# Performance work log

Measured on AMD Instinct MI355X. Metric: run time of the kernel, lower is better.

Reference implementation:

```python
import jax, jax.numpy as jnp
import numpy as np

B, S, H, V, T, NS, NB, NSW = 16, 200, 400, 25000, 8, 30, 3, 36


def setup_inputs() -> dict:
    key = jax.random.key(0)
    ks = jax.random.split(key, 12)
    return {
        "encoded_hidden": jax.random.normal(ks[0], (1, B, H), jnp.float32),
        "encoded_outputs": jax.random.normal(ks[1], (B, S, H), jnp.float32),
        "story": jax.random.randint(ks[2], (B, S), 0, V),
        "target_batches": jax.random.randint(ks[3], (B, NS, T), 0, V),
        "slot_dom_idx": jax.random.randint(ks[4], (NS,), 0, NSW),
        "slot_slot_idx": jax.random.randint(ks[5], (NS,), 0, NSW),
        "emb_W": jax.random.normal(ks[6], (V, H), jnp.float32) * 0.05,
        "slot_emb_W": jax.random.normal(ks[7], (NSW, H), jnp.float32) * 0.1,
        "gru_W_ih": jax.random.normal(ks[8], (3 * H, H), jnp.float32) * 0.05,
        "gru_W_hh": jax.random.normal(ks[9], (3 * H, H), jnp.float32) * 0.05,
        "gru_b_ih": jnp.zeros((3 * H,), jnp.float32),
        "gru_b_hh": jnp.zeros((3 * H,), jnp.float32),
        "W_ratio_w": jax.random.normal(ks[10], (1, 3 * H), jnp.float32) * 0.05,
        "W_ratio_b": jnp.zeros((1,), jnp.float32),
        "W_gate_w": jax.random.normal(ks[11], (NB, H), jnp.float32) * 0.05,
        "W_gate_b": jnp.zeros((NB,), jnp.float32),
    }


def reference(encoded_hidden, encoded_outputs, story, target_batches,
              slot_dom_idx, slot_slot_idx, emb_W, slot_emb_W,
              gru_W_ih, gru_W_hh, gru_b_ih, gru_b_hh,
              W_ratio_w, W_ratio_b, W_gate_w, W_gate_b):
    b, s, h = encoded_outputs.shape
    ns = slot_dom_idx.shape[0]
    v = emb_W.shape[0]
    t = target_batches.shape[2]
    bs = ns * b  # flattened slot*batch dim (parallel decode over slots)

    # slot embedding = domain_emb + slot_emb, broadcast over batch
    slot_emb = slot_emb_W[slot_dom_idx] + slot_emb_W[slot_slot_idx]        # [ns,h]
    dec_in0 = jnp.broadcast_to(slot_emb[:, None, :], (ns, b, h)).reshape(bs, h)
    h0 = jnp.tile(encoded_hidden[0], (ns, 1))                              # [bs,h]
    enc = jnp.tile(encoded_outputs, (ns, 1, 1))                            # [bs,s,h]
    pad_mask = jnp.tile(story == 0, (ns, 1))                               # [bs,s]
    story_rep = jnp.tile(story, (ns, 1))                                   # [bs,s]
    # teacher forcing targets, slot-major flatten: [bs, t]
    tf = jnp.transpose(target_batches, (1, 0, 2)).reshape(bs, t)
    rows = jnp.arange(bs)

    def gru_cell(x, hid):
        gx = x @ gru_W_ih.T + gru_b_ih
        gh = hid @ gru_W_hh.T + gru_b_hh
        r = jax.nn.sigmoid(gx[:, :h] + gh[:, :h])
        z = jax.nn.sigmoid(gx[:, h:2 * h] + gh[:, h:2 * h])
        n = jnp.tanh(gx[:, 2 * h:] + r * gh[:, 2 * h:])
        return (1.0 - z) * n + z * hid

    def step(carry, tgt_t):
        hid, x = carry
        hid = gru_cell(x, hid)                                             # [bs,h]
        scores = jnp.einsum('bh,bsh->bs', hid, enc)
        scores = jnp.where(pad_mask, -jnp.inf, scores)
        prob = jax.nn.softmax(scores, axis=1)                              # [bs,s]
        ctx = jnp.einsum('bs,bsh->bh', prob, enc)                          # [bs,h]
        p_vocab = jax.nn.softmax(hid @ emb_W.T, axis=1)                    # [bs,v]
        switch = jax.nn.sigmoid(
            jnp.concatenate([hid, ctx, x], axis=-1) @ W_ratio_w.T + W_ratio_b)  # [bs,1]
        p_ctx = jnp.zeros((bs, v), p_vocab.dtype).at[rows[:, None], story_rep].add(prob)
        final = (1.0 - switch) * p_ctx + switch * p_vocab                  # [bs,v]
        x_next = emb_W[tgt_t]                                              # teacher forcing
        return (hid, x_next), (final, ctx)

    (_, _), (finals, ctxs) = jax.lax.scan(step, (h0, dec_in0), tf.T)
    all_point = jnp.transpose(finals.reshape(t, ns, b, v), (1, 2, 0, 3))   # [ns,b,t,v]
    all_gate = (ctxs[0] @ W_gate_w.T + W_gate_b).reshape(ns, b, -1)        # [ns,b,nb_gate]
    return all_point, all_gate
```

## Files before the change

### kernel.cpp

```cpp
#include <hip/hip_runtime.h>
#include <math.h>

#define B_   16
#define S_   200
#define H_   400
#define V_   25000
#define T_   8
#define NS_  30
#define NB_  3
#define NSW_ 36
#define BS_  480

#define KP_  448
#define MP_  512
#define NP_  25088
#define NG_  1280
#define MA_  3840
#define NVT_ (NP_/128)
#define PSL_ 200

typedef unsigned short u16;
typedef __attribute__((ext_vector_type(4))) float f32x4;
typedef __attribute__((ext_vector_type(8))) short short8;

__device__ __forceinline__ u16 f2bf(float f) {
    unsigned u = __float_as_uint(f);
    u += 0x7FFFu + ((u >> 16) & 1u);
    return (u16)(u >> 16);
}
__device__ __forceinline__ float bf2f(u16 v) {
    return __uint_as_float(((unsigned)v) << 16);
}
__device__ __forceinline__ float wred_sum(float v) {
    v += __shfl_xor(v, 32); v += __shfl_xor(v, 16); v += __shfl_xor(v, 8);
    v += __shfl_xor(v, 4);  v += __shfl_xor(v, 2);  v += __shfl_xor(v, 1);
    return v;
}
__device__ __forceinline__ float wred_max(float v) {
    v = fmaxf(v, __shfl_xor(v, 32)); v = fmaxf(v, __shfl_xor(v, 16));
    v = fmaxf(v, __shfl_xor(v, 8));  v = fmaxf(v, __shfl_xor(v, 4));
    v = fmaxf(v, __shfl_xor(v, 2));  v = fmaxf(v, __shfl_xor(v, 1));
    return v;
}

__device__ __forceinline__ void gload_lds16(const void* g, void* l) {
    __builtin_amdgcn_global_load_lds(
        (const __attribute__((address_space(1))) void*)g,
        (__attribute__((address_space(3))) void*)l, 16, 0, 0);
}

#define MFMA_SETUP()                                                          \
    const int wid = tid >> 6, lane = tid & 63;                                \
    const int wr = wid >> 1, wc = wid & 1;                                    \
    f32x4 acc[4][4] = {};                                                     \
    const int sslot = lane & 7;                                               \
    const int srow8 = (lane >> 3) & 7;                                        \
    const int lcol = (sslot ^ srow8) * 8;                                     \
    const int lr = lane & 15, lg = lane >> 4, lx = lane & 7;                  \
    const int sA0 = (lg ^ lx) * 8, sA1 = ((4 + lg) ^ lx) * 8;

#define STAGE_TILE(k0_)                                                       \
    {                                                                         \
        _Pragma("unroll")                                                     \
        for (int is = 0; is < 4; ++is) {                                      \
            gload_lds16(Ag + (size_t)is * 8 * KP_ + (k0_),                    \
                        &As[(wid * 32 + is * 8) * 64]);                       \
            gload_lds16(Bg + (size_t)is * 8 * KP_ + (k0_),                    \
                        &Bs[(wid * 32 + is * 8) * 64]);                       \
        }                                                                     \
    }

#define COMPUTE_TILE()                                                        \
    {                                                                         \
        short8 af[4][2], bfr[4][2];                                           \
        _Pragma("unroll")                                                     \
        for (int i = 0; i < 4; ++i) {                                         \
            int ra = (wr * 64 + i * 16 + lr) * 64;                            \
            af[i][0] = *reinterpret_cast<const short8*>(&As[ra + sA0]);       \
            af[i][1] = *reinterpret_cast<const short8*>(&As[ra + sA1]);       \
            int rb = (wc * 64 + i * 16 + lr) * 64;                            \
            bfr[i][0] = *reinterpret_cast<const short8*>(&Bs[rb + sA0]);      \
            bfr[i][1] = *reinterpret_cast<const short8*>(&Bs[rb + sA1]);      \
        }                                                                     \
        _Pragma("unroll")                                                     \
        for (int h = 0; h < 2; ++h)                                           \
            _Pragma("unroll")                                                 \
            for (int i = 0; i < 4; ++i)                                       \
                _Pragma("unroll")                                             \
                for (int j = 0; j < 4; ++j)                                   \
                    acc[i][j] = __builtin_amdgcn_mfma_f32_16x16x32_bf16(      \
                        af[i][h], bfr[j][h], acc[i][j], 0, 0, 0);             \
    }

#define MFMA_KLOOP_SB()                                                       \
    _Pragma("unroll")                                                         \
    for (int kt = 0; kt < 7; ++kt) {                                          \
        STAGE_TILE(kt * 64);                                                  \
        __syncthreads();                                                      \
        COMPUTE_TILE();                                                       \
        __syncthreads();                                                      \
    }

__global__ void init_all(const float* __restrict__ eh, float* __restrict__ hid,
                         u16* __restrict__ Ab) {
    int i = blockIdx.x * blockDim.x + threadIdx.x;
    if (i >= MP_ * KP_) return;
    int row = i / KP_, d = i - row * KP_;
    u16 v = 0;
    if (row < BS_ && d < H_) {
        float h = eh[(row % B_) * H_ + d];
        hid[row * H_ + d] = h;
        v = f2bf(h);
    }
    Ab[i] = v;
}

__device__ __forceinline__ void conv_chunk(const float* __restrict__ src,
                                           u16* __restrict__ dst, int i, int rows) {
    int row = i / (KP_ / 8), c8 = (i - row * (KP_ / 8)) * 8;
    short8 o = {};
    if (row < rows && c8 < H_) {
        const float4* s = reinterpret_cast<const float4*>(src + (size_t)row * H_ + c8);
        float4 a = s[0], b = s[1];
        o[0] = (short)f2bf(a.x); o[1] = (short)f2bf(a.y);
        o[2] = (short)f2bf(a.z); o[3] = (short)f2bf(a.w);
        o[4] = (short)f2bf(b.x); o[5] = (short)f2bf(b.y);
        o[6] = (short)f2bf(b.z); o[7] = (short)f2bf(b.w);
    }
    *reinterpret_cast<short8*>(dst + (size_t)row * KP_ + c8) = o;
}

__global__ void conv_all(const float* __restrict__ embW, const float* __restrict__ Wih,
                         const float* __restrict__ Whh, u16* __restrict__ Bb,
                         u16* __restrict__ Wihb, u16* __restrict__ Whhb) {
    const int CB = NP_ * (KP_ / 8), CG = NG_ * (KP_ / 8);
    int i = blockIdx.x * blockDim.x + threadIdx.x;
    if (i < CB) conv_chunk(embW, Bb, i, V_);
    else if (i < CB + CG) conv_chunk(Wih, Wihb, i - CB, 3 * H_);
    else if (i < CB + 2 * CG) conv_chunk(Whh, Whhb, i - CB - CG, 3 * H_);
}

__global__ void xall_prep(const int* __restrict__ tb, const float* __restrict__ embW,
                          const float* __restrict__ sembW,
                          const int* __restrict__ dom, const int* __restrict__ sli,
                          float* __restrict__ x_all, u16* __restrict__ Xb_all) {
    int i = blockIdx.x * blockDim.x + threadIdx.x;
    if (i >= MA_ * (KP_ / 8)) return;
    int row = i / (KP_ / 8), c8 = (i - row * (KP_ / 8)) * 8;
    int t = row / BS_, r = row - t * BS_;
    int batch = r % B_, slot = r / B_;
    short8 o = {};
    if (c8 < H_) {
        float4 a, b;
        if (t == 0) {
            const float4* s0 = reinterpret_cast<const float4*>(sembW + dom[slot] * H_ + c8);
            const float4* s1 = reinterpret_cast<const float4*>(sembW + sli[slot] * H_ + c8);
            float4 x0 = s0[0], x1 = s0[1], y0 = s1[0], y1 = s1[1];
            a = make_float4(x0.x + y0.x, x0.y + y0.y, x0.z + y0.z, x0.w + y0.w);
            b = make_float4(x1.x + y1.x, x1.y + y1.y, x1.z + y1.z, x1.w + y1.w);
        } else {
            int tok = tb[(batch * NS_ + slot) * T_ + (t - 1)];
            const float4* s = reinterpret_cast<const float4*>(embW + (size_t)tok * H_ + c8);
            a = s[0]; b = s[1];
        }
        o[0] = (short)f2bf(a.x); o[1] = (short)f2bf(a.y);
        o[2] = (short)f2bf(a.z); o[3] = (short)f2bf(a.w);
        o[4] = (short)f2bf(b.x); o[5] = (short)f2bf(b.y);
        o[6] = (short)f2bf(b.z); o[7] = (short)f2bf(b.w);
        *reinterpret_cast<float4*>(x_all + (size_t)row * H_ + c8) = a;
        *reinterpret_cast<float4*>(x_all + (size_t)row * H_ + c8 + 4) = b;
    }
    *reinterpret_cast<short8*>(Xb_all + (size_t)row * KP_ + c8) = o;
}

__global__ __launch_bounds__(256)
void gemm_setup(const u16* __restrict__ Xb_all, const u16* __restrict__ Abuf,
                const u16* __restrict__ Wihb, const u16* __restrict__ Whhb,
                float* __restrict__ gx_all, float* __restrict__ gh) {
    __shared__ u16 As[128 * 64];
    __shared__ u16 Bs[128 * 64];
    const int tid = threadIdx.x;
    const bool mainp = blockIdx.y < (MA_ / 128);
    const int m0 = (mainp ? blockIdx.y : blockIdx.y - MA_ / 128) * 128;
    const int n0 = blockIdx.x * 128;
    const u16* A = mainp ? Xb_all : Abuf;
    const u16* Bw = mainp ? Wihb : Whhb;
    float* C = mainp ? gx_all : gh;
    const int Mlim = mainp ? MA_ : BS_;

    MFMA_SETUP();
    const u16* Ag = A + (size_t)(m0 + wid * 32 + (lane >> 3)) * KP_ + lcol;
    const u16* Bg = Bw + (size_t)(n0 + wid * 32 + (lane >> 3)) * KP_ + lcol;
    MFMA_KLOOP_SB();

    const int m_base = m0 + wr * 64 + lg * 4;
    const int n_base = n0 + wc * 64 + lr;
    #pragma unroll
    for (int i = 0; i < 4; ++i)
        #pragma unroll
        for (int r = 0; r < 4; ++r) {
            int m = m_base + i * 16 + r;
            if (m >= Mlim) continue;
            #pragma unroll
            for (int j = 0; j < 4; ++j) {
                int n = n_base + j * 16;
                if (n < 3 * H_) C[(size_t)m * 3 * H_ + n] = acc[i][j][r];
            }
        }
}

__global__ __launch_bounds__(256)
void vocab_gh(const u16* __restrict__ A, const u16* __restrict__ Bb,
              const u16* __restrict__ Whhb, u16* __restrict__ pb_cur,
              float* __restrict__ psum_cur, float* __restrict__ gh,
              const u16* __restrict__ pb_prev, const float* __restrict__ psum_prev,
              const float* __restrict__ sw_prev, const float* __restrict__ prob_prev,
              const int* __restrict__ story, float* __restrict__ out,
              int t, int do_fin) {
    __shared__ u16 As[128 * 64];
    __shared__ u16 Bs[128 * 64];
    __shared__ float sred[2][128];
    const int bid = blockIdx.x;
    const int tid = threadIdx.x;

    if (do_fin && t > 0 && bid < BS_) {
        const int row = bid, batch = row % B_;
        const int w = tid >> 6, l = tid & 63;
        float rs = (tid < NVT_) ? psum_prev[(size_t)row * PSL_ + tid] : 0.f;
        rs = wred_sum(rs);
        if (l == 0) sred[0][w] = rs;
        __syncthreads();
        float denom = sred[0][0] + sred[0][1] + sred[0][2] + sred[0][3];
        float swv = sw_prev[row];
        float scl = swv / denom;
        const u16* ps = pb_prev + (size_t)row * V_;
        float* p = out + ((size_t)row * T_ + (t - 1)) * V_;
        for (int v = tid * 8; v < V_; v += 256 * 8) {
            short8 in = *reinterpret_cast<const short8*>(ps + v);
            float4 o0, o1;
            o0.x = bf2f((u16)in[0]) * scl; o0.y = bf2f((u16)in[1]) * scl;
            o0.z = bf2f((u16)in[2]) * scl; o0.w = bf2f((u16)in[3]) * scl;
            o1.x = bf2f((u16)in[4]) * scl; o1.y = bf2f((u16)in[5]) * scl;
            o1.z = bf2f((u16)in[6]) * scl; o1.w = bf2f((u16)in[7]) * scl;
            *reinterpret_cast<float4*>(p + v) = o0;
            *reinterpret_cast<float4*>(p + v + 4) = o1;
        }
        __syncthreads();
        float om = 1.f - swv;
        for (int s = tid; s < S_; s += 256) {
            int tok = story[batch * S_ + s];
            atomicAdd(p + tok, om * prob_prev[(size_t)row * S_ + s]);
        }
        __syncthreads();
    }

    const int lin = (bid & 7) * 103 + (bid >> 3);
    const int ntall = lin >> 2, mt = lin & 3;
    const bool isv = (ntall < NVT_);
    const int n0 = (isv ? ntall : ntall - NVT_) * 128;
    const int m0 = mt * 128;
    const u16* Bsrc = isv ? Bb : Whhb;

    MFMA_SETUP();
    const u16* Ag = A + (size_t)(m0 + wid * 32 + (lane >> 3)) * KP_ + lcol;
    const u16* Bg = Bsrc + (size_t)(n0 + wid * 32 + (lane >> 3)) * KP_ + lcol;
    MFMA_KLOOP_SB();

    const int m_base = m0 + wr * 64 + lg * 4;
    const int n_base = n0 + wc * 64 + lr;
    if (isv) {
        #pragma unroll
        for (int i = 0; i < 4; ++i) {
            #pragma unroll
            for (int r = 0; r < 4; ++r) {
                int m = m_base + i * 16 + r;
                float js = 0.f;
                #pragma unroll
                for (int j = 0; j < 4; ++j) {
                    int n = n_base + j * 16;
                    float e = __expf(acc[i][j][r]);
                    if (m < BS_ && n < V_) {
                        pb_cur[(size_t)m * V_ + n] = f2bf(e);
                        js += e;
                    }
                }
                js += __shfl_xor(js, 1);
                js += __shfl_xor(js, 2);
                js += __shfl_xor(js, 4);
                js += __shfl_xor(js, 8);
                if ((lane & 15) == 0) sred[wc][m - m0] = js;
            }
        }
        __syncthreads();
        if (tid < 128) {
            int m = m0 + tid;
            psum_cur[(size_t)m * PSL_ + ntall] = sred[0][tid] + sred[1][tid];
        }
    } else {
        #pragma unroll
        for (int i = 0; i < 4; ++i)
            #pragma unroll
            for (int r = 0; r < 4; ++r) {
                int m = m_base + i * 16 + r;
                if (m >= BS_) continue;
                #pragma unroll
                for (int j = 0; j < 4; ++j) {
                    int n = n_base + j * 16;
                    if (n < 3 * H_) gh[(size_t)m * 3 * H_ + n] = acc[i][j][r];
                }
            }
    }
}

__global__ __launch_bounds__(256)
void attn_fused(const float* __restrict__ gx_all, const float* __restrict__ gh,
                const float* __restrict__ bih, const float* __restrict__ bhh,
                float* __restrict__ hid, u16* __restrict__ Ab,
                const float* __restrict__ x_all,
                const float* __restrict__ enc, const int* __restrict__ story,
                const float* __restrict__ Wr, const float* __restrict__ Wrb,
                const float* __restrict__ Wg, const float* __restrict__ Wgb,
                float* __restrict__ prob_cur, float* __restrict__ sw_cur,
                float* __restrict__ gate_out,
                float* __restrict__ out, const u16* __restrict__ pb_prev,
                const float* __restrict__ psum_prev, const float* __restrict__ sw_prev,
                const float* __restrict__ prob_prev, int t, int do_fin) {
    const int bid = blockIdx.x;
    const int lin = (bid & 7) * 60 + (bid >> 3);
    const int batch = lin / 30, slot = lin - batch * 30;
    const int row = slot * B_ + batch;
    const int tid = threadIdx.x, w = tid >> 6, l = tid & 63;
    __shared__ __align__(16) float hs[H_];
    __shared__ __align__(16) float xs[H_];
    __shared__ __align__(16) float cs[H_];
    __shared__ float sc[S_];
    __shared__ float red[16];

    if (do_fin && t > 0) {
        float rs = (tid < NVT_) ? psum_prev[(size_t)row * PSL_ + tid] : 0.f;
        rs = wred_sum(rs);
        if (l == 0) red[w] = rs;
        __syncthreads();
        float denom = red[0] + red[1] + red[2] + red[3];
        float swv = sw_prev[row];
        float scl = swv / denom;
        const u16* ps = pb_prev + (size_t)row * V_;
        float* p = out + ((size_t)row * T_ + (t - 1)) * V_;
        for (int v = tid * 8; v < V_; v += 256 * 8) {
            short8 in = *reinterpret_cast<const short8*>(ps + v);
            float4 o0, o1;
            o0.x = bf2f((u16)in[0]) * scl; o0.y = bf2f((u16)in[1]) * scl;
            o0.z = bf2f((u16)in[2]) * scl; o0.w = bf2f((u16)in[3]) * scl;
            o1.x = bf2f((u16)in[4]) * scl; o1.y = bf2f((u16)in[5]) * scl;
            o1.z = bf2f((u16)in[6]) * scl; o1.w = bf2f((u16)in[7]) * scl;
            *reinterpret_cast<float4*>(p + v) = o0;
            *reinterpret_cast<float4*>(p + v + 4) = o1;
        }
        __syncthreads();
        float om = 1.f - swv;
        for (int s = tid; s < S_; s += 256) {
            int tok = story[batch * S_ + s];
            atomicAdd(p + tok, om * prob_prev[(size_t)row * S_ + s]);
        }
        __syncthreads();
    }

    const float* gxr = gx_all + ((size_t)t * BS_ + row) * 3 * H_;
    const float* ghr = gh + (size_t)row * 3 * H_;
    const float* xr  = x_all + ((size_t)t * BS_ + row) * H_;
    for (int d = tid; d < H_; d += 256) {
        float r = 1.f / (1.f + expf(-(gxr[d] + bih[d] + ghr[d] + bhh[d])));
        float z = 1.f / (1.f + expf(-(gxr[H_ + d] + bih[H_ + d] + ghr[H_ + d] + bhh[H_ + d])));
        float n = tanhf(gxr[2 * H_ + d] + bih[2 * H_ + d] + r * (ghr[2 * H_ + d] + bhh[2 * H_ + d]));
        float h = (1.f - z) * n + z * hid[(size_t)row * H_ + d];
        hs[d] = h;
        hid[(size_t)row * H_ + d] = h;
        Ab[(size_t)row * KP_ + d] = f2bf(h);
        xs[d] = xr[d];
    }
    __syncthreads();

    const float* encb = enc + (size_t)batch * S_ * H_;
    {
        float4 hv1 = *reinterpret_cast<const float4*>(&hs[l * 4]);
        float4 hv2 = make_float4(0.f, 0.f, 0.f, 0.f);
        if (l < 36) hv2 = *reinterpret_cast<const float4*>(&hs[256 + l * 4]);
        for (int k = 0; k < 50; ++k) {
            int s = w * 50 + k;
            const float4* e = reinterpret_cast<const float4*>(encb + (size_t)s * H_);
            float4 ev = e[l];
            float part = ev.x * hv1.x + ev.y * hv1.y + ev.z * hv1.z + ev.w * hv1.w;
            if (l < 36) {
                float4 ev2 = e[64 + l];
                part += ev2.x * hv2.x + ev2.y * hv2.y + ev2.z * hv2.z + ev2.w * hv2.w;
            }
            part = wred_sum(part);
            if (l == 0)
                sc[s] = (story[batch * S_ + s] == 0) ? -1e30f : part;
        }
    }
    __syncthreads();

    float v = (tid < S_) ? sc[tid] : -1e30f;
    float wm = wred_max(v);
    if (l == 0) red[w] = wm;
    __syncthreads();
    float mx = fmaxf(fmaxf(red[0], red[1]), fmaxf(red[2], red[3]));
    float e = (tid < S_) ? __expf(v - mx) : 0.f;
    float wsum = wred_sum(e);
    if (l == 0) red[4 + w] = wsum;
    __syncthreads();
    float inv = 1.f / (red[4] + red[5] + red[6] + red[7]);
    if (tid < S_) {
        float pv = e * inv;
        sc[tid] = pv;
        prob_cur[(size_t)row * S_ + tid] = pv;
    }
    __syncthreads();

    for (int d = tid; d < H_; d += 256) {
        float a0 = 0.f, a1 = 0.f;
        for (int s = 0; s < S_; s += 2) {
            a0 += sc[s] * encb[(size_t)s * H_ + d];
            a1 += sc[s + 1] * encb[(size_t)(s + 1) * H_ + d];
        }
        cs[d] = a0 + a1;
    }
    __syncthreads();

    float part = 0.f;
    for (int i = tid; i < 3 * H_; i += 256) {
        float xv = (i < H_) ? hs[i] : (i < 2 * H_) ? cs[i - H_] : xs[i - 2 * H_];
        part += xv * Wr[i];
    }
    part = wred_sum(part);
    if (l == 0) red[8 + w] = part;
    __syncthreads();
    if (tid == 0)
        sw_cur[row] = 1.f / (1.f + expf(-(red[8] + red[9] + red[10] + red[11] + Wrb[0])));

    if (t == 0 && tid < NB_) {
        float acc = 0.f;
        for (int d = 0; d < H_; ++d) acc += cs[d] * Wg[tid * H_ + d];
        gate_out[(size_t)row * NB_ + tid] = acc + Wgb[tid];
    }
}

__global__ __launch_bounds__(256)
void scale_scatter(float* __restrict__ out, const u16* __restrict__ pb,
                   const float* __restrict__ psum, const float* __restrict__ sw,
                   const float* __restrict__ prob, const int* __restrict__ story) {
    const int row = blockIdx.x;
    const int tid = threadIdx.x, w = tid >> 6, l = tid & 63;
    __shared__ float red[4];
    float rs = (tid < NVT_) ? psum[(size_t)row * PSL_ + tid] : 0.f;
    rs = wred_sum(rs);
    if (l == 0) red[w] = rs;
    __syncthreads();
    float denom = red[0] + red[1] + red[2] + red[3];
    float swv = sw[row];
    float scl = swv / denom;
    const u16* ps = pb + (size_t)row * V_;
    float* p = out + ((size_t)row * T_ + (T_ - 1)) * V_;
    for (int v = tid * 8; v < V_; v += 256 * 8) {
        short8 in = *reinterpret_cast<const short8*>(ps + v);
        float4 o0, o1;
        o0.x = bf2f((u16)in[0]) * scl; o0.y = bf2f((u16)in[1]) * scl;
        o0.z = bf2f((u16)in[2]) * scl; o0.w = bf2f((u16)in[3]) * scl;
        o1.x = bf2f((u16)in[4]) * scl; o1.y = bf2f((u16)in[5]) * scl;
        o1.z = bf2f((u16)in[6]) * scl; o1.w = bf2f((u16)in[7]) * scl;
        *reinterpret_cast<float4*>(p + v) = o0;
        *reinterpret_cast<float4*>(p + v + 4) = o1;
    }
    __syncthreads();
    const int batch = row % B_;
    float om = 1.f - swv;
    for (int s = tid; s < S_; s += 256) {
        int tok = story[batch * S_ + s];
        atomicAdd(p + tok, om * prob[(size_t)row * S_ + s]);
    }
}

extern "C" void kernel_launch(void* const* d_in, const int* in_sizes, int n_in,
                              void* d_out, int out_size, void* d_ws, size_t ws_size,
                              hipStream_t stream) {
    const float* eh    = (const float*)d_in[0];
    const float* enc   = (const float*)d_in[1];
    const int*   story = (const int*)d_in[2];
    const int*   tb    = (const int*)d_in[3];
    const int*   dom   = (const int*)d_in[4];
    const int*   sli   = (const int*)d_in[5];
    const float* embW  = (const float*)d_in[6];
    const float* sembW = (const float*)d_in[7];
    const float* Wih   = (const float*)d_in[8];
    const float* Whh   = (const float*)d_in[9];
    const float* bih   = (const float*)d_in[10];
    const float* bhh   = (const float*)d_in[11];
    const float* Wr    = (const float*)d_in[12];
    const float* Wrb   = (const float*)d_in[13];
    const float* Wg    = (const float*)d_in[14];
    const float* Wgb   = (const float*)d_in[15];

    float* out = (float*)d_out;
    float* ws  = (float*)d_ws;

    float* gx_all = ws;
    float* gh     = gx_all + (size_t)MA_ * 3 * H_;
    float* hid    = gh + (size_t)BS_ * 3 * H_;
    float* x_all  = hid + (size_t)BS_ * H_;
    float* prob2  = x_all + (size_t)MA_ * H_;
    float* sw2    = prob2 + 2 * BS_ * S_;
    float* psum2  = sw2 + 2 * BS_;
    u16* Ab     = (u16*)(psum2 + 2 * (size_t)MP_ * PSL_);
    u16* Xb_all = Ab + (size_t)MP_ * KP_;
    u16* Wihb   = Xb_all + (size_t)MA_ * KP_;
    u16* Whhb   = Wihb + (size_t)NG_ * KP_;
    u16* Bb     = Whhb + (size_t)NG_ * KP_;
    u16* pb0    = Bb + (size_t)NP_ * KP_;
    u16* pb1    = pb0 + (size_t)BS_ * V_;
    size_t need_base = (size_t)((char*)pb1 - (char*)ws);
    size_t need_full = (size_t)((char*)(pb1 + (size_t)BS_ * V_) - (char*)ws);
    if (ws_size < need_base) return;
    const int dbl = (ws_size >= need_full) ? 1 : 0;

    float* gate_out = out + (size_t)NS_ * B_ * T_ * V_;

    init_all<<<(MP_ * KP_ + 255) / 256, 256, 0, stream>>>(eh, hid, Ab);
    {
        int tot = (NP_ + 2 * NG_) * (KP_ / 8);
        conv_all<<<(tot + 255) / 256, 256, 0, stream>>>(embW, Wih, Whh, Bb, Wihb, Whhb);
    }
    xall_prep<<<(MA_ * (KP_ / 8) + 255) / 256, 256, 0, stream>>>(tb, embW, sembW, dom, sli,
                                                                 x_all, Xb_all);
    gemm_setup<<<dim3(NG_ / 128, MA_ / 128 + MP_ / 128), 256, 0, stream>>>(
        Xb_all, Ab, Wihb, Whhb, gx_all, gh);

    for (int t = 0; t < T_; ++t) {
        const int cur = t & 1, prev = cur ^ 1;
        float* prob_cur = prob2 + cur * BS_ * S_;
        float* prob_prev = prob2 + prev * BS_ * S_;
        float* sw_cur = sw2 + cur * BS_;
        float* sw_prev = sw2 + prev * BS_;
        float* psum_cur = psum2 + (size_t)cur * MP_ * PSL_;
        float* psum_prev = psum2 + (size_t)prev * MP_ * PSL_;
        u16* pb_cur = dbl ? (cur ? pb1 : pb0) : pb0;
        u16* pb_prev = dbl ? (prev ? pb1 : pb0) : pb0;

        attn_fused<<<BS_, 256, 0, stream>>>(gx_all, gh, bih, bhh, hid, Ab, x_all,
                                            enc, story, Wr, Wrb, Wg, Wgb,
                                            prob_cur, sw_cur, gate_out,
                                            out, pb_prev, psum_prev, sw_prev, prob_prev,
                                            t, dbl ? 0 : 1);
        vocab_gh<<<824, 256, 0, stream>>>(Ab, Bb, Whhb, pb_cur, psum_cur, gh,
                                          pb_prev, psum_prev, sw_prev, prob_prev,
                                          story, out, t, dbl);
    }
    {
        const int last = (T_ - 1) & 1;
        scale_scatter<<<BS_, 256, 0, stream>>>(out, dbl ? (last ? pb1 : pb0) : pb0,
                                               psum2 + (size_t)last * MP_ * PSL_,
                                               sw2 + last * BS_,
                                               prob2 + last * BS_ * S_, story);
    }
}
```

Measured before the change: 807.0 us.

## Move finalize into attention kernel, enlarge vocab GEMM M-tile, single-buffer probs

The vocab/gh GEMM now uses 256x128 tiles (2 M tiles instead of 4), so each block loads a B (embedding) tile once for twice as many rows and the grid halves to 412 blocks, with launch bounds asking for 2 blocks per CU. The finalize step for the previous timestep (scale plus scatter-add into the output) moves from the vocab kernel into a combined attention/finalize launch of 960 blocks, where odd blocks do finalize and even blocks do attention. Because finalize of step t-1 now runs before the vocab GEMM of step t overwrites pb, the double-buffered pb/psum arrays are removed, cutting workspace. The larger tile raises register pressure from 128 accumulators per thread. The single-stage k-loop with a sync on every iteration may also expose more load latency.

Result: faster. 777.9 us (-3.6%).

```diff
diff --git a/kernel.cpp b/kernel.cpp
--- a/kernel.cpp
+++ b/kernel.cpp
@@ -209,31 +209,144 @@
         }
 }
 
-__global__ __launch_bounds__(256)
+__global__ __launch_bounds__(256, 2)
 void vocab_gh(const u16* __restrict__ A, const u16* __restrict__ Bb,
-              const u16* __restrict__ Whhb, u16* __restrict__ pb_cur,
-              float* __restrict__ psum_cur, float* __restrict__ gh,
-              const u16* __restrict__ pb_prev, const float* __restrict__ psum_prev,
-              const float* __restrict__ sw_prev, const float* __restrict__ prob_prev,
-              const int* __restrict__ story, float* __restrict__ out,
-              int t, int do_fin) {
-    __shared__ u16 As[128 * 64];
+              const u16* __restrict__ Whhb, u16* __restrict__ pb,
+              float* __restrict__ psum, float* __restrict__ gh) {
+    __shared__ u16 As[256 * 64];
     __shared__ u16 Bs[128 * 64];
-    __shared__ float sred[2][128];
+    __shared__ float sred[2][256];
     const int bid = blockIdx.x;
     const int tid = threadIdx.x;
-
-    if (do_fin && t > 0 && bid < BS_) {
-        const int row = bid, batch = row % B_;
-        const int w = tid >> 6, l = tid & 63;
-        float rs = (tid < NVT_) ? psum_prev[(size_t)row * PSL_ + tid] : 0.f;
+    const int xcd = bid & 7, idx = bid >> 3;
+    const int lin = (xcd < 4) ? (xcd * 52 + idx) : (208 + (xcd - 4) * 51 + idx);
+    const int ntall = lin >> 1, mt = lin & 1;
+    const bool isv = (ntall < NVT_);
+    const int n0 = (isv ? ntall : ntall - NVT_) * 128;
+    const int m0 = mt * 256;
+    const u16* Bsrc = isv ? Bb : Whhb;
+
+    const int wid = tid >> 6, lane = tid & 63;
+    const int wr = wid >> 1, wc = wid & 1;
+    f32x4 acc[8][4] = {};
+    const int sslot = lane & 7;
+    const int srow8 = (lane >> 3) & 7;
+    const int lcol = (sslot ^ srow8) * 8;
+    const int lr = lane & 15, lg = lane >> 4, lx = lane & 7;
+    const int sA0 = (lg ^ lx) * 8, sA1 = ((4 + lg) ^ lx) * 8;
+
+    const u16* Ag = A + (size_t)(m0 + wid * 64 + (lane >> 3)) * KP_ + lcol;
+    const u16* Bg = Bsrc + (size_t)(n0 + wid * 32 + (lane >> 3)) * KP_ + lcol;
+
+    for (int kt = 0; kt < 7; ++kt) {
+        const int k0 = kt * 64;
+        #pragma unroll
+        for (int is = 0; is < 8; ++is)
+            gload_lds16(Ag + (size_t)is * 8 * KP_ + k0, &As[(wid * 64 + is * 8) * 64]);
+        #pragma unroll
+        for (int is = 0; is < 4; ++is)
+            gload_lds16(Bg + (size_t)is * 8 * KP_ + k0, &Bs[(wid * 32 + is * 8) * 64]);
+        __syncthreads();
+        #pragma unroll
+        for (int h = 0; h < 2; ++h) {
+            const int sA = h ? sA1 : sA0;
+            short8 af[8], bf[4];
+            #pragma unroll
+            for (int i = 0; i < 8; ++i)
+                af[i] = *reinterpret_cast<const short8*>(&As[(wr * 128 + i * 16 + lr) * 64 + sA]);
+            #pragma unroll
+            for (int j = 0; j < 4; ++j)
+                bf[j] = *reinterpret_cast<const short8*>(&Bs[(wc * 64 + j * 16 + lr) * 64 + sA]);
+            #pragma unroll
+            for (int i = 0; i < 8; ++i)
+                #pragma unroll
+                for (int j = 0; j < 4; ++j)
+                    acc[i][j] = __builtin_amdgcn_mfma_f32_16x16x32_bf16(
+                        af[i], bf[j], acc[i][j], 0, 0, 0);
+        }
+        __syncthreads();
+    }
+
+    const int m_base = m0 + wr * 128 + lg * 4;
+    const int n_base = n0 + wc * 64 + lr;
+    if (isv) {
+        #pragma unroll
+        for (int i = 0; i < 8; ++i) {
+            #pragma unroll
+            for (int r = 0; r < 4; ++r) {
+                int m = m_base + i * 16 + r;
+                float js = 0.f;
+                #pragma unroll
+                for (int j = 0; j < 4; ++j) {
+                    int n = n_base + j * 16;
+                    float e = __expf(acc[i][j][r]);
+                    if (m < BS_ && n < V_) {
+                        pb[(size_t)m * V_ + n] = f2bf(e);
+                        js += e;
+                    }
+                }
+                js += __shfl_xor(js, 1);
+                js += __shfl_xor(js, 2);
+                js += __shfl_xor(js, 4);
+                js += __shfl_xor(js, 8);
+                if ((lane & 15) == 0) sred[wc][m - m0] = js;
+            }
+        }
+        __syncthreads();
+        {
+            int m = m0 + tid;
+            psum[(size_t)m * PSL_ + ntall] = sred[0][tid] + sred[1][tid];
+        }
+    } else {
+        #pragma unroll
+        for (int i = 0; i < 8; ++i)
+            #pragma unroll
+            for (int r = 0; r < 4; ++r) {
+                int m = m_base + i * 16 + r;
+                if (m >= BS_) continue;
+                #pragma unroll
+                for (int j = 0; j < 4; ++j) {
+                    int n = n_base + j * 16;
+                    if (n < 3 * H_) gh[(size_t)m * 3 * H_ + n] = acc[i][j][r];
+                }
+            }
+    }
+}
+
+__global__ __launch_bounds__(256)
+void attn_fin(const float* __restrict__ gx_all, const float* __restrict__ gh,
+              const float* __restrict__ bih, const float* __restrict__ bhh,
+              float* __restrict__ hid, u16* __restrict__ Ab,
+              const float* __restrict__ x_all,
+              const float* __restrict__ enc, const int* __restrict__ story,
+              const float* __restrict__ Wr, const float* __restrict__ Wrb,
+              const float* __restrict__ Wg, const float* __restrict__ Wgb,
+              float* __restrict__ prob_cur, float* __restrict__ sw_cur,
+              float* __restrict__ gate_out,
+              float* __restrict__ out, const u16* __restrict__ pb,
+              const float* __restrict__ psum, const float* __restrict__ sw_prev,
+              const float* __restrict__ prob_prev, int t) {
+    const int bid = blockIdx.x;
+    const int lin = (bid & 7) * 120 + (bid >> 3);
+    const int work = lin >> 1, kind = lin & 1;
+    const int tid = threadIdx.x, w = tid >> 6, l = tid & 63;
+    __shared__ __align__(16) float hs[H_];
+    __shared__ __align__(16) float xs[H_];
+    __shared__ __align__(16) float cs[H_];
+    __shared__ float sc[S_];
+    __shared__ float red[16];
+
+    if (kind == 1) {
+        if (t == 0) return;
+        const int row = work, batch = row % B_;
+        float rs = (tid < NVT_) ? psum[(size_t)row * PSL_ + tid] : 0.f;
         rs = wred_sum(rs);
-        if (l == 0) sred[0][w] = rs;
+        if (l == 0) red[w] = rs;
         __syncthreads();
-        float denom = sred[0][0] + sred[0][1] + sred[0][2] + sred[0][3];
+        float denom = red[0] + red[1] + red[2] + red[3];
         float swv = sw_prev[row];
         float scl = swv / denom;
-        const u16* ps = pb_prev + (size_t)row * V_;
+        const u16* ps = pb + (size_t)row * V_;
         float* p = out + ((size_t)row * T_ + (t - 1)) * V_;
         for (int v = tid * 8; v < V_; v += 256 * 8) {
             short8 in = *reinterpret_cast<const short8*>(ps + v);
@@ -251,119 +364,11 @@
             int tok = story[batch * S_ + s];
             atomicAdd(p + tok, om * prob_prev[(size_t)row * S_ + s]);
         }
-        __syncthreads();
-    }
-
-    const int lin = (bid & 7) * 103 + (bid >> 3);
-    const int ntall = lin >> 2, mt = lin & 3;
-    const bool isv = (ntall < NVT_);
-    const int n0 = (isv ? ntall : ntall - NVT_) * 128;
-    const int m0 = mt * 128;
-    const u16* Bsrc = isv ? Bb : Whhb;
-
-    MFMA_SETUP();
-    const u16* Ag = A + (size_t)(m0 + wid * 32 + (lane >> 3)) * KP_ + lcol;
-    const u16* Bg = Bsrc + (size_t)(n0 + wid * 32 + (lane >> 3)) * KP_ + lcol;
-    MFMA_KLOOP_SB();
-
-    const int m_base = m0 + wr * 64 + lg * 4;
-    const int n_base = n0 + wc * 64 + lr;
-    if (isv) {
-        #pragma unroll
-        for (int i = 0; i < 4; ++i) {
-            #pragma unroll
-            for (int r = 0; r < 4; ++r) {
-                int m = m_base + i * 16 + r;
-                float js = 0.f;
-                #pragma unroll
-                for (int j = 0; j < 4; ++j) {
-                    int n = n_base + j * 16;
-                    float e = __expf(acc[i][j][r]);
-                    if (m < BS_ && n < V_) {
-                        pb_cur[(size_t)m * V_ + n] = f2bf(e);
-                        js += e;
-                    }
-                }
-                js += __shfl_xor(js, 1);
-                js += __shfl_xor(js, 2);
-                js += __shfl_xor(js, 4);
-                js += __shfl_xor(js, 8);
-                if ((lane & 15) == 0) sred[wc][m - m0] = js;
-            }
-        }
-        __syncthreads();
-        if (tid < 128) {
-            int m = m0 + tid;
-            psum_cur[(size_t)m * PSL_ + ntall] = sred[0][tid] + sred[1][tid];
-        }
-    } else {
-        #pragma unroll
-        for (int i = 0; i < 4; ++i)
-            #pragma unroll
-            for (int r = 0; r < 4; ++r) {
-                int m = m_base + i * 16 + r;
-                if (m >= BS_) continue;
-                #pragma unroll
-                for (int j = 0; j < 4; ++j) {
-                    int n = n_base + j * 16;
-                    if (n < 3 * H_) gh[(size_t)m * 3 * H_ + n] = acc[i][j][r];
-                }
-            }
-    }
-}
-
-__global__ __launch_bounds__(256)
-void attn_fused(const float* __restrict__ gx_all, const float* __restrict__ gh,
-                const float* __restrict__ bih, const float* __restrict__ bhh,
-                float* __restrict__ hid, u16* __restrict__ Ab,
-                const float* __restrict__ x_all,
-                const float* __restrict__ enc, const int* __restrict__ story,
-                const float* __restrict__ Wr, const float* __restrict__ Wrb,
-                const float* __restrict__ Wg, const float* __restrict__ Wgb,
-                float* __restrict__ prob_cur, float* __restrict__ sw_cur,
-                float* __restrict__ gate_out,
-                float* __restrict__ out, const u16* __restrict__ pb_prev,
-                const float* __restrict__ psum_prev, const float* __restrict__ sw_prev,
-                const float* __restrict__ prob_prev, int t, int do_fin) {
-    const int bid = blockIdx.x;
-    const int lin = (bid & 7) * 60 + (bid >> 3);
-    const int batch = lin / 30, slot = lin - batch * 30;
+        return;
+    }
+
+    const int batch = work / 30, slot = work - batch * 30;
     const int row = slot * B_ + batch;
-    const int tid = threadIdx.x, w = tid >> 6, l = tid & 63;
-    __shared__ __align__(16) float hs[H_];
-    __shared__ __align__(16) float xs[H_];
-    __shared__ __align__(16) float cs[H_];
-    __shared__ float sc[S_];
-    __shared__ float red[16];
-
-    if (do_fin && t > 0) {
-        float rs = (tid < NVT_) ? psum_prev[(size_t)row * PSL_ + tid] : 0.f;
-        rs = wred_sum(rs);
-        if (l == 0) red[w] = rs;
-        __syncthreads();
-        float denom = red[0] + red[1] + red[2] + red[3];
-        float swv = sw_prev[row];
-        float scl = swv / denom;
-        const u16* ps = pb_prev + (size_t)row * V_;
-        float* p = out + ((size_t)row * T_ + (t - 1)) * V_;
-        for (int v = tid * 8; v < V_; v += 256 * 8) {
-            short8 in = *reinterpret_cast<const short8*>(ps + v);
-            float4 o0, o1;
-            o0.x = bf2f((u16)in[0]) * scl; o0.y = bf2f((u16)in[1]) * scl;
-            o0.z = bf2f((u16)in[2]) * scl; o0.w = bf2f((u16)in[3]) * scl;
-            o1.x = bf2f((u16)in[4]) * scl; o1.y = bf2f((u16)in[5]) * scl;
-            o1.z = bf2f((u16)in[6]) * scl; o1.w = bf2f((u16)in[7]) * scl;
-            *reinterpret_cast<float4*>(p + v) = o0;
-            *reinterpret_cast<float4*>(p + v + 4) = o1;
-        }
-        __syncthreads();
-        float om = 1.f - swv;
-        for (int s = tid; s < S_; s += 256) {
-            int tok = story[batch * S_ + s];
-            atomicAdd(p + tok, om * prob_prev[(size_t)row * S_ + s]);
-        }
-        __syncthreads();
-    }
 
     const float* gxr = gx_all + ((size_t)t * BS_ + row) * 3 * H_;
     const float* ghr = gh + (size_t)row * 3 * H_;
@@ -510,18 +515,15 @@
     float* x_all  = hid + (size_t)BS_ * H_;
     float* prob2  = x_all + (size_t)MA_ * H_;
     float* sw2    = prob2 + 2 * BS_ * S_;
-    float* psum2  = sw2 + 2 * BS_;
-    u16* Ab     = (u16*)(psum2 + 2 * (size_t)MP_ * PSL_);
+    float* psum   = sw2 + 2 * BS_;
+    u16* Ab     = (u16*)(psum + (size_t)MP_ * PSL_);
     u16* Xb_all = Ab + (size_t)MP_ * KP_;
     u16* Wihb   = Xb_all + (size_t)MA_ * KP_;
     u16* Whhb   = Wihb + (size_t)NG_ * KP_;
     u16* Bb     = Whhb + (size_t)NG_ * KP_;
-    u16* pb0    = Bb + (size_t)NP_ * KP_;
-    u16* pb1    = pb0 + (size_t)BS_ * V_;
-    size_t need_base = (size_t)((char*)pb1 - (char*)ws);
-    size_t need_full = (size_t)((char*)(pb1 + (size_t)BS_ * V_) - (char*)ws);
-    if (ws_size < need_base) return;
-    const int dbl = (ws_size >= need_full) ? 1 : 0;
+    u16* pb     = Bb + (size_t)NP_ * KP_;
+    size_t need = (size_t)((char*)(pb + (size_t)BS_ * V_) - (char*)ws);
+    if (ws_size < need) return;
 
     float* gate_out = out + (size_t)NS_ * B_ * T_ * V_;
 
@@ -537,29 +539,16 @@
 
     for (int t = 0; t < T_; ++t) {
         const int cur = t & 1, prev = cur ^ 1;
-        float* prob_cur = prob2 + cur * BS_ * S_;
-        float* prob_prev = prob2 + prev * BS_ * S_;
-        float* sw_cur = sw2 + cur * BS_;
-        float* sw_prev = sw2 + prev * BS_;
-        float* psum_cur = psum2 + (size_t)cur * MP_ * PSL_;
-        float* psum_prev = psum2 + (size_t)prev * MP_ * PSL_;
-        u16* pb_cur = dbl ? (cur ? pb1 : pb0) : pb0;
-        u16* pb_prev = dbl ? (prev ? pb1 : pb0) : pb0;
-
-        attn_fused<<<BS_, 256, 0, stream>>>(gx_all, gh, bih, bhh, hid, Ab, x_all,
-                                            enc, story, Wr, Wrb, Wg, Wgb,
-                                            prob_cur, sw_cur, gate_out,
-                                            out, pb_prev, psum_prev, sw_prev, prob_prev,
-                                            t, dbl ? 0 : 1);
-        vocab_gh<<<824, 256, 0, stream>>>(Ab, Bb, Whhb, pb_cur, psum_cur, gh,
-                                          pb_prev, psum_prev, sw_prev, prob_prev,
-                                          story, out, t, dbl);
+        attn_fin<<<960, 256, 0, stream>>>(gx_all, gh, bih, bhh, hid, Ab, x_all,
+                                          enc, story, Wr, Wrb, Wg, Wgb,
+                                          prob2 + cur * BS_ * S_, sw2 + cur * BS_,
+                                          gate_out, out, pb, psum,
+                                          sw2 + prev * BS_, prob2 + prev * BS_ * S_, t);
+        vocab_gh<<<412, 256, 0, stream>>>(Ab, Bb, Whhb, pb, psum, gh);
     }
     {
         const int last = (T_ - 1) & 1;
-        scale_scatter<<<BS_, 256, 0, stream>>>(out, dbl ? (last ? pb1 : pb0) : pb0,
-                                               psum2 + (size_t)last * MP_ * PSL_,
-                                               sw2 + last * BS_,
+        scale_scatter<<<BS_, 256, 0, stream>>>(out, pb, psum, sw2 + last * BS_,
                                                prob2 + last * BS_ * S_, story);
     }
 }
```
